# Kernel optimization log

Hardware: AMD Instinct MI355X
Metric: run time of the kernel (lower is better)

## Reference

```python
import jax, jax.numpy as jnp
import numpy as np

B, N, M = 1, 3000, 3000        # surface points, query points
K = N + M                       # nodes per graph
IN, HID, H, OUT = 3, 64, 4, 2   # in_channels, hidden_channels, heads, out_channels
RADIUS2 = 0.05 ** 2
NEG_SLOPE = 0.2
NEG_INF = jnp.float32(-1e9)


def setup_inputs() -> dict:
    key = jax.random.key(0)
    ks = jax.random.split(key, 12)
    s1 = 1.0 / np.sqrt(IN)
    s2 = 1.0 / np.sqrt(H * HID)
    return {
        "pos": jax.random.uniform(ks[0], (B, 3, N), dtype=jnp.float32),
        "pos_non_manifold": jax.random.uniform(ks[1], (B, 3, M), dtype=jnp.float32),
        # GAT layer 1: lin weight, attention vectors (per head), bias
        "W1": jax.random.normal(ks[2], (IN, H * HID), dtype=jnp.float32) * s1,
        "a_src1": jax.random.normal(ks[3], (H, HID), dtype=jnp.float32) * s2,
        "a_dst1": jax.random.normal(ks[4], (H, HID), dtype=jnp.float32) * s2,
        "b1": jnp.zeros((H * HID,), dtype=jnp.float32),
        # GAT layer 2
        "W2": jax.random.normal(ks[5], (H * HID, H * HID), dtype=jnp.float32) * s2,
        "a_src2": jax.random.normal(ks[6], (H, HID), dtype=jnp.float32) * s2,
        "a_dst2": jax.random.normal(ks[7], (H, HID), dtype=jnp.float32) * s2,
        "b2": jnp.zeros((H * HID,), dtype=jnp.float32),
        # final fc
        "fc_w": jax.random.normal(ks[8], (H * HID, OUT), dtype=jnp.float32) * s2,
        "fc_b": jnp.zeros((OUT,), dtype=jnp.float32),
    }


def _gat_layer(x, mask, W, a_src, a_dst, b):
    # x: [B,K,Fin]; mask: [B,K,K] (mask[b,i,j] True if edge j->i, symmetric, incl. diag)
    h = (x @ W).reshape(x.shape[0], x.shape[1], H, HID)        # [B,K,H,C]
    es = jnp.einsum('bjhc,hc->bjh', h, a_src)                   # source score
    ed = jnp.einsum('bihc,hc->bih', h, a_dst)                   # destination score
    e = ed[:, :, None, :] + es[:, None, :, :]                   # [B,i,j,H]
    e = jnp.where(e >= 0, e, NEG_SLOPE * e)                     # LeakyReLU(0.2)
    e = jnp.where(mask[..., None], e, NEG_INF)
    alpha = jax.nn.softmax(e, axis=2)                           # softmax over sources j
    out = jnp.einsum('bijh,bjhc->bihc', alpha, h)               # [B,K,H,C]
    return out.reshape(x.shape[0], x.shape[1], H * HID) + b


def reference(pos, pos_non_manifold, W1, a_src1, a_dst1, b1,
              W2, a_src2, a_dst2, b2, fc_w, fc_b):
    # cat along point dim then transpose -> [B, K, 3]
    pts = jnp.concatenate([pos, pos_non_manifold], axis=2).transpose(0, 2, 1)
    # squared cdist via gram trick (avoids [B,K,K,3] intermediate)
    sq = jnp.sum(pts * pts, axis=-1)                            # [B,K]
    d2 = sq[:, :, None] + sq[:, None, :] - 2.0 * jnp.einsum('bid,bjd->bij', pts, pts)
    mask = d2 < RADIUS2                                         # adjacency (block-diag per batch)
    x = jax.nn.relu(_gat_layer(pts, mask, W1, a_src1, a_dst1, b1))
    x = jax.nn.relu(_gat_layer(x, mask, W2, a_src2, a_dst2, b2))
    x = x @ fc_w + fc_b                                         # [B,K,OUT]
    # original: x[:, num_points:].reshape(B, OUT, 3000) with num_points = M
    logits = x[:, M:].reshape(pts.shape[0], OUT, 3000)
    return logits
```

## Files before the change

### kernel.cpp

```cpp
#include <hip/hip_runtime.h>

#define NPTS   3000
#define MPTS   3000
#define KNODES 6000
#define HEADS  4
#define FDIM   256
#define OUTC   2
#define R2     0.0025f
#define NSLOPE 0.2f
#define MAXNBR 64
#define RPB    8

#define GDIM   16
#define NCELL  4096
#define CAP    16
#define POISON 0xAAAAAAAAu

#define OFF_ES2  0
#define OFF_ED2  24000
#define OFF_H2   48000
#define OFF_END  1584000

__device__ __forceinline__ float wsum(float v) {
#pragma unroll
    for (int off = 32; off; off >>= 1) v += __shfl_xor(v, off, 64);
    return v;
}

__global__ void k_grid(const float* __restrict__ pos, const float* __restrict__ pnm,
                       unsigned* __restrict__ cellcnt, float4* __restrict__ bucket) {
    int i = blockIdx.x * 256 + threadIdx.x;
    if (i >= KNODES) return;
    float x, y, z;
    if (i < NPTS) { x = pos[i]; y = pos[NPTS + i]; z = pos[2 * NPTS + i]; }
    else { int q = i - NPTS; x = pnm[q]; y = pnm[MPTS + q]; z = pnm[2 * MPTS + q]; }
    int cx = min((int)(x * 16.f), 15);
    int cy = min((int)(y * 16.f), 15);
    int cz = min((int)(z * 16.f), 15);
    int cell = (cz << 8) | (cy << 4) | cx;
    unsigned slot = atomicAdd(&cellcnt[cell], 1u) - POISON;
    if (slot < CAP)
        bucket[cell * CAP + slot] = make_float4(x, y, z, __int_as_float(i));
}

__global__ __launch_bounds__(256) void k_main(
        const float* __restrict__ pos, const float* __restrict__ pnm,
        const float* __restrict__ W1, const float* __restrict__ as1,
        const float* __restrict__ ad1, const float* __restrict__ b1,
        const float* __restrict__ W2, const float* __restrict__ as2,
        const float* __restrict__ ad2,
        const unsigned* __restrict__ cellcnt, const float4* __restrict__ bucket,
        float* __restrict__ h2, float* __restrict__ es2, float* __restrict__ ed2,
        int* __restrict__ cnt, int* __restrict__ idx) {
    __shared__ int   s_cnt[RPB];
    __shared__ int   s_idx[MAXNBR][RPB];
    __shared__ float s_nx[MAXNBR][RPB], s_ny[MAXNBR][RPB], s_nz[MAXNBR][RPB];
    __shared__ float s_u[HEADS][3], s_v[HEADS][3];
    __shared__ float s_q[RPB][HEADS][3];
    __shared__ __align__(16) float xs[RPB][FDIM];
    const int t = threadIdx.x;
    const int lane = t & 63;
    const int i0 = blockIdx.x * RPB;
    if (t < RPB) s_cnt[t] = 0;

    const float w1a = W1[t], w1b = W1[FDIM + t], w1c = W1[2 * FDIM + t];
    {
        const float asv = as1[t], adv = ad1[t];
        float u0 = wsum(w1a * asv), u1 = wsum(w1b * asv), u2 = wsum(w1c * asv);
        float v0 = wsum(w1a * adv), v1 = wsum(w1b * adv), v2 = wsum(w1c * adv);
        if (lane == 0) {
            int h = t >> 6;
            s_u[h][0] = u0; s_u[h][1] = u1; s_u[h][2] = u2;
            s_v[h][0] = v0; s_v[h][1] = v1; s_v[h][2] = v2;
        }
    }

    const float* base = (i0 < NPTS) ? pos : pnm;
    const int ib = (i0 < NPTS) ? i0 : i0 - NPTS;
    float xi[RPB], yi[RPB], zi[RPB], si[RPB];
#pragma unroll
    for (int r = 0; r < RPB; ++r) {
        float px = base[ib + r], py = base[NPTS + ib + r], pz = base[2 * NPTS + ib + r];
        xi[r] = px; yi[r] = py; zi[r] = pz;
        si[r] = __fadd_rn(__fadd_rn(__fmul_rn(px, px), __fmul_rn(py, py)),
                          __fmul_rn(pz, pz));
    }
    __syncthreads();

    {
        const int r = t >> 5, l32 = t & 31;
        if (l32 < 27) {
            int cx = min((int)(xi[r] * 16.f), 15);
            int cy = min((int)(yi[r] * 16.f), 15);
            int cz = min((int)(zi[r] * 16.f), 15);
            int dx = l32 % 3 - 1, dy = (l32 / 3) % 3 - 1, dz = l32 / 9 - 1;
            int nx_ = cx + dx, ny_ = cy + dy, nz_ = cz + dz;
            if (((nx_ | ny_ | nz_) >= 0) && nx_ < 16 && ny_ < 16 && nz_ < 16) {
                int cell = (nz_ << 8) | (ny_ << 4) | nx_;
                unsigned n = min(cellcnt[cell] - POISON, (unsigned)CAP);
                for (unsigned e = 0; e < n; ++e) {
                    float4 pj = bucket[cell * CAP + e];
                    float sj = __fadd_rn(__fadd_rn(__fmul_rn(pj.x, pj.x),
                                                   __fmul_rn(pj.y, pj.y)),
                                         __fmul_rn(pj.z, pj.z));
                    float dot = __fadd_rn(__fadd_rn(__fmul_rn(xi[r], pj.x),
                                                    __fmul_rn(yi[r], pj.y)),
                                          __fmul_rn(zi[r], pj.z));
                    float d2 = __fsub_rn(__fadd_rn(si[r], sj), __fmul_rn(2.0f, dot));
                    if (d2 < R2) {
                        int p = atomicAdd(&s_cnt[r], 1);
                        if (p < MAXNBR) {
                            s_idx[p][r] = __float_as_int(pj.w);
                            s_nx[p][r] = pj.x; s_ny[p][r] = pj.y; s_nz[p][r] = pj.z;
                        }
                    }
                }
            }
        }
    }
    __syncthreads();
    if (i0 >= NPTS) {
        if (t < RPB) cnt[i0 + t] = min(s_cnt[t], MAXNBR);
#pragma unroll
        for (int r = 0; r < RPB; ++r) {
            int c = min(s_cnt[r], MAXNBR);
            if (t < c) idx[(i0 + r) * MAXNBR + t] = s_idx[t][r];
        }
    }

    if (t < 64) {
        const int pr = (t & 31) >> 2, h = t & 3;
        const int c = min(s_cnt[pr], MAXNBR);
        const float u0 = s_u[h][0], u1 = s_u[h][1], u2 = s_u[h][2];
        const float dsum = fmaf(xi[pr], s_v[h][0],
                           fmaf(yi[pr], s_v[h][1], zi[pr] * s_v[h][2]));
        float m = -1e30f;
        for (int jl = 0; jl < c; ++jl) {
            float e = dsum + fmaf(s_nx[jl][pr], u0,
                             fmaf(s_ny[jl][pr], u1, s_nz[jl][pr] * u2));
            e = (e >= 0.f) ? e : NSLOPE * e;
            m = fmaxf(m, e);
        }
        float S = 0.f, q0 = 0.f, q1 = 0.f, q2 = 0.f;
        for (int jl = 0; jl < c; ++jl) {
            float xj = s_nx[jl][pr], yj = s_ny[jl][pr], zj = s_nz[jl][pr];
            float e = dsum + fmaf(xj, u0, fmaf(yj, u1, zj * u2));
            e = (e >= 0.f) ? e : NSLOPE * e;
            float a = __expf(e - m);
            S += a;
            q0 = fmaf(a, xj, q0); q1 = fmaf(a, yj, q1); q2 = fmaf(a, zj, q2);
        }
        if (t < 32) {
            float inv = 1.f / S;
            s_q[pr][h][0] = q0 * inv;
            s_q[pr][h][1] = q1 * inv;
            s_q[pr][h][2] = q2 * inv;
        }
    }
    __syncthreads();

    {
        const float b1v = b1[t];
        const int h = t >> 6;
#pragma unroll
        for (int r = 0; r < RPB; ++r) {
            float q0 = s_q[r][h][0], q1 = s_q[r][h][1], q2 = s_q[r][h][2];
            float v = fmaf(q0, w1a, fmaf(q1, w1b, q2 * w1c)) + b1v;
            xs[r][t] = fmaxf(v, 0.f);
        }
    }
    __syncthreads();

    {
        const int tl = t & 127, halfb = t >> 7;
        const int rbase = halfb * 4;
        float acc0[4], acc1[4];
#pragma unroll
        for (int r = 0; r < 4; ++r) { acc0[r] = 0.f; acc1[r] = 0.f; }
        const float2* Wp = (const float2*)W2;
#pragma unroll 4
        for (int k4 = 0; k4 < FDIM / 4; ++k4) {
            float2 w0 = Wp[(4 * k4 + 0) * 128 + tl];
            float2 w1 = Wp[(4 * k4 + 1) * 128 + tl];
            float2 w2 = Wp[(4 * k4 + 2) * 128 + tl];
            float2 w3 = Wp[(4 * k4 + 3) * 128 + tl];
#pragma unroll
            for (int r = 0; r < 4; ++r) {
                float4 xv = ((const float4*)xs[rbase + r])[k4];
                acc0[r] = fmaf(xv.x, w0.x, fmaf(xv.y, w1.x,
                          fmaf(xv.z, w2.x, fmaf(xv.w, w3.x, acc0[r]))));
                acc1[r] = fmaf(xv.x, w0.y, fmaf(xv.y, w1.y,
                          fmaf(xv.z, w2.y, fmaf(xv.w, w3.y, acc1[r]))));
            }
        }
        const int c0 = 2 * tl;
#pragma unroll
        for (int r = 0; r < 4; ++r) {
            int row = i0 + rbase + r;
            *(float2*)&h2[(size_t)row * FDIM + c0] = make_float2(acc0[r], acc1[r]);
        }
        const float as0 = as2[c0], as1v = as2[c0 + 1];
        const float ad0 = ad2[c0], ad1v = ad2[c0 + 1];
        const int hh = tl >> 5;
#pragma unroll
        for (int r = 0; r < 4; ++r) {
            int row = i0 + rbase + r;
            float s = fmaf(acc0[r], as0, acc1[r] * as1v);
            float d = fmaf(acc0[r], ad0, acc1[r] * ad1v);
#pragma unroll
            for (int off = 16; off; off >>= 1) {
                s += __shfl_down(s, off, 64);
                d += __shfl_down(d, off, 64);
            }
            if ((lane & 31) == 0) {
                es2[row * HEADS + hh] = s;
                ed2[row * HEADS + hh] = d;
            }
        }
    }
}

__global__ void k_agg2fc(const float* __restrict__ h, const float* __restrict__ es,
                         const float* __restrict__ ed, const int* __restrict__ cnt,
                         const int* __restrict__ idx, const float* __restrict__ bias,
                         const float* __restrict__ fw, const float* __restrict__ fb,
                         float* __restrict__ out) {
    __shared__ int   s_idx[MAXNBR];
    __shared__ float s_e[MAXNBR * HEADS];
    __shared__ float s_ed[HEADS];
    __shared__ float s_red[8];
    int q = blockIdx.x;
    int i = MPTS + q;
    int t = threadIdx.x;
    int c = cnt[i];
    if (t < c) s_idx[t] = idx[i * MAXNBR + t];
    if (t < HEADS) s_ed[t] = ed[i * HEADS + t];
    __syncthreads();
    if (t < c * HEADS) {
        int jl = t >> 2, hh = t & 3;
        float e = s_ed[hh] + es[s_idx[jl] * HEADS + hh];
        e = (e >= 0.f) ? e : NSLOPE * e;
        s_e[jl * HEADS + hh] = e;
    }
    __syncthreads();
    int hh = t >> 6;
    float m = -1e30f;
    for (int jl = 0; jl < c; ++jl) m = fmaxf(m, s_e[jl * HEADS + hh]);
    float ssum = 0.f, acc = 0.f;
    for (int jl = 0; jl < c; ++jl) {
        float p = __expf(s_e[jl * HEADS + hh] - m);
        ssum += p;
        acc = fmaf(p, h[s_idx[jl] * FDIM + t], acc);
    }
    float v = fmaxf(acc / ssum + bias[t], 0.f);
    float p0 = v * fw[t * OUTC + 0];
    float p1 = v * fw[t * OUTC + 1];
    for (int off = 32; off; off >>= 1) {
        p0 += __shfl_down(p0, off, 64);
        p1 += __shfl_down(p1, off, 64);
    }
    if ((t & 63) == 0) {
        s_red[(t >> 6) * 2 + 0] = p0;
        s_red[(t >> 6) * 2 + 1] = p1;
    }
    __syncthreads();
    if (t == 0) {
        out[q * OUTC + 0] = s_red[0] + s_red[2] + s_red[4] + s_red[6] + fb[0];
        out[q * OUTC + 1] = s_red[1] + s_red[3] + s_red[5] + s_red[7] + fb[1];
    }
}

extern "C" void kernel_launch(void* const* d_in, const int* in_sizes, int n_in,
                              void* d_out, int out_size, void* d_ws, size_t ws_size,
                              hipStream_t stream) {
    const float* pos   = (const float*)d_in[0];
    const float* pnm   = (const float*)d_in[1];
    const float* W1    = (const float*)d_in[2];
    const float* asrc1 = (const float*)d_in[3];
    const float* adst1 = (const float*)d_in[4];
    const float* b1    = (const float*)d_in[5];
    const float* W2    = (const float*)d_in[6];
    const float* asrc2 = (const float*)d_in[7];
    const float* adst2 = (const float*)d_in[8];
    const float* b2    = (const float*)d_in[9];
    const float* fcw   = (const float*)d_in[10];
    const float* fcb   = (const float*)d_in[11];
    float* out = (float*)d_out;

    float* w    = (float*)d_ws;
    float* es2  = w + OFF_ES2;
    float* ed2  = w + OFF_ED2;
    float* h2   = w + OFF_H2;
    int* nbr_cnt = (int*)((char*)d_ws + (size_t)4 * OFF_END);
    int* nbr_idx = nbr_cnt + KNODES;
    unsigned* cellcnt = (unsigned*)(nbr_idx + (size_t)KNODES * MAXNBR);
    float4* bucket = (float4*)(cellcnt + NCELL);

    k_grid<<<(KNODES + 255) / 256, 256, 0, stream>>>(pos, pnm, cellcnt, bucket);
    k_main<<<KNODES / RPB, 256, 0, stream>>>(pos, pnm, W1, asrc1, adst1, b1,
                                             W2, asrc2, adst2, cellcnt, bucket,
                                             h2, es2, ed2, nbr_cnt, nbr_idx);
    k_agg2fc<<<MPTS, FDIM, 0, stream>>>(h2, es2, ed2, nbr_cnt, nbr_idx, b2,
                                        fcw, fcb, out);
}
```

Measured before the change: 119.0 us.

## Stage W2 tiles through shared memory with register prefetch in layer-2 GEMM

The layer-2 linear transform now copies W2 in 32 KB chunks into a shared buffer, which aliases the neighbour-list arrays. It does this cooperatively with float4 loads, prefetching the next chunk into registers while the current one is consumed. Previously each thread read W2 float2 values directly from global memory. The aim is coalesced wide loads and overlap of global latency with FMAs. The cost is extra barriers per chunk, 32 register float4s of prefetch state, and more LDS, which may lower occupancy.

```diff
diff --git a/kernel.cpp b/kernel.cpp
--- a/kernel.cpp
+++ b/kernel.cpp
@@ -52,12 +52,15 @@
         const unsigned* __restrict__ cellcnt, const float4* __restrict__ bucket,
         float* __restrict__ h2, float* __restrict__ es2, float* __restrict__ ed2,
         int* __restrict__ cnt, int* __restrict__ idx) {
+    __shared__ __align__(16) float smem[8192];
     __shared__ int   s_cnt[RPB];
-    __shared__ int   s_idx[MAXNBR][RPB];
-    __shared__ float s_nx[MAXNBR][RPB], s_ny[MAXNBR][RPB], s_nz[MAXNBR][RPB];
     __shared__ float s_u[HEADS][3], s_v[HEADS][3];
     __shared__ float s_q[RPB][HEADS][3];
     __shared__ __align__(16) float xs[RPB][FDIM];
+    int*   s_idx = (int*)smem;
+    float* s_nx  = smem + 512;
+    float* s_ny  = smem + 1024;
+    float* s_nz  = smem + 1536;
     const int t = threadIdx.x;
     const int lane = t & 63;
     const int i0 = blockIdx.x * RPB;
@@ -110,8 +113,10 @@
                     if (d2 < R2) {
                         int p = atomicAdd(&s_cnt[r], 1);
                         if (p < MAXNBR) {
-                            s_idx[p][r] = __float_as_int(pj.w);
-                            s_nx[p][r] = pj.x; s_ny[p][r] = pj.y; s_nz[p][r] = pj.z;
+                            s_idx[p * RPB + r] = __float_as_int(pj.w);
+                            s_nx[p * RPB + r] = pj.x;
+                            s_ny[p * RPB + r] = pj.y;
+                            s_nz[p * RPB + r] = pj.z;
                         }
                     }
                 }
@@ -124,7 +129,7 @@
 #pragma unroll
         for (int r = 0; r < RPB; ++r) {
             int c = min(s_cnt[r], MAXNBR);
-            if (t < c) idx[(i0 + r) * MAXNBR + t] = s_idx[t][r];
+            if (t < c) idx[(i0 + r) * MAXNBR + t] = s_idx[t * RPB + r];
         }
     }
 
@@ -136,14 +141,15 @@
                            fmaf(yi[pr], s_v[h][1], zi[pr] * s_v[h][2]));
         float m = -1e30f;
         for (int jl = 0; jl < c; ++jl) {
-            float e = dsum + fmaf(s_nx[jl][pr], u0,
-                             fmaf(s_ny[jl][pr], u1, s_nz[jl][pr] * u2));
+            float e = dsum + fmaf(s_nx[jl * RPB + pr], u0,
+                             fmaf(s_ny[jl * RPB + pr], u1, s_nz[jl * RPB + pr] * u2));
             e = (e >= 0.f) ? e : NSLOPE * e;
             m = fmaxf(m, e);
         }
         float S = 0.f, q0 = 0.f, q1 = 0.f, q2 = 0.f;
         for (int jl = 0; jl < c; ++jl) {
-            float xj = s_nx[jl][pr], yj = s_ny[jl][pr], zj = s_nz[jl][pr];
+            float xj = s_nx[jl * RPB + pr], yj = s_ny[jl * RPB + pr],
+                  zj = s_nz[jl * RPB + pr];
             float e = dsum + fmaf(xj, u0, fmaf(yj, u1, zj * u2));
             e = (e >= 0.f) ? e : NSLOPE * e;
             float a = __expf(e - m);
@@ -169,28 +175,47 @@
             xs[r][t] = fmaxf(v, 0.f);
         }
     }
-    __syncthreads();
 
     {
         const int tl = t & 127, halfb = t >> 7;
         const int rbase = halfb * 4;
+        float4* wbuf4 = (float4*)smem;
+        const float2* wbuf2 = (const float2*)smem;
         float acc0[4], acc1[4];
 #pragma unroll
         for (int r = 0; r < 4; ++r) { acc0[r] = 0.f; acc1[r] = 0.f; }
-        const float2* Wp = (const float2*)W2;
-#pragma unroll 4
-        for (int k4 = 0; k4 < FDIM / 4; ++k4) {
-            float2 w0 = Wp[(4 * k4 + 0) * 128 + tl];
-            float2 w1 = Wp[(4 * k4 + 1) * 128 + tl];
-            float2 w2 = Wp[(4 * k4 + 2) * 128 + tl];
-            float2 w3 = Wp[(4 * k4 + 3) * 128 + tl];
-#pragma unroll
-            for (int r = 0; r < 4; ++r) {
-                float4 xv = ((const float4*)xs[rbase + r])[k4];
-                acc0[r] = fmaf(xv.x, w0.x, fmaf(xv.y, w1.x,
-                          fmaf(xv.z, w2.x, fmaf(xv.w, w3.x, acc0[r]))));
-                acc1[r] = fmaf(xv.x, w0.y, fmaf(xv.y, w1.y,
-                          fmaf(xv.z, w2.y, fmaf(xv.w, w3.y, acc1[r]))));
+        float4 tmp[8];
+        {
+            const float4* Wg = (const float4*)W2;
+#pragma unroll
+            for (int q = 0; q < 8; ++q) tmp[q] = Wg[q * 256 + t];
+        }
+#pragma unroll 1
+        for (int kb = 0; kb < 8; ++kb) {
+            __syncthreads();
+#pragma unroll
+            for (int q = 0; q < 8; ++q) wbuf4[q * 256 + t] = tmp[q];
+            __syncthreads();
+            if (kb < 7) {
+                const float4* Wg = (const float4*)(W2 + (kb + 1) * 8192);
+#pragma unroll
+                for (int q = 0; q < 8; ++q) tmp[q] = Wg[q * 256 + t];
+            }
+#pragma unroll
+            for (int k4l = 0; k4l < 8; ++k4l) {
+                const int k4 = (kb << 3) + k4l;
+                float2 w0 = wbuf2[(4 * k4l + 0) * 128 + tl];
+                float2 w1 = wbuf2[(4 * k4l + 1) * 128 + tl];
+                float2 w2 = wbuf2[(4 * k4l + 2) * 128 + tl];
+                float2 w3 = wbuf2[(4 * k4l + 3) * 128 + tl];
+#pragma unroll
+                for (int r = 0; r < 4; ++r) {
+                    float4 xv = ((const float4*)xs[rbase + r])[k4];
+                    acc0[r] = fmaf(xv.x, w0.x, fmaf(xv.y, w1.x,
+                              fmaf(xv.z, w2.x, fmaf(xv.w, w3.x, acc0[r]))));
+                    acc1[r] = fmaf(xv.x, w0.y, fmaf(xv.y, w1.y,
+                              fmaf(xv.z, w2.y, fmaf(xv.w, w3.y, acc1[r]))));
+                }
             }
         }
         const int c0 = 2 * tl;
```

Result: slower. 152.0 us (+27.8%).
